# Kernel optimization log

Measured on AMD Instinct MI355X. Metric: run time of the kernel, lower is better.

## Reference

```python
import jax, jax.numpy as jnp
import numpy as np

D = 512
F = 2048
H = 8
L = 128
B = 4


def _layer_norm(x, g, b, eps=1e-5):
    mu = jnp.mean(x, axis=-1, keepdims=True)
    var = jnp.var(x, axis=-1, keepdims=True)
    return (x - mu) * jax.lax.rsqrt(var + eps) * g + b


def _edge_mlp(Q, arc, W, b, arc_is_middle_out):
    # Equivalent to relu(Linear(concat(A, arc, B_))) with W: (3D, D), without
    # materializing the (B,L,L,3D) concat: split W into three D-blocks.
    # For W_out: concat(h_bf, arc, h_bf_t) -> block1 acts on Q[b,i], block3 on Q[b,j].
    # For W_in:  concat(h_bf_t, arc, h_bf) -> block1 acts on Q[b,j], block3 on Q[b,i].
    d = Q.shape[-1]
    W1, W2, W3 = W[:d], W[d:2 * d], W[2 * d:]
    mid = jnp.einsum('bijd,de->bije', arc, W2)
    if arc_is_middle_out:  # W_out ordering
        left = jnp.einsum('bid,de->bie', Q, W1)[:, :, None, :]   # broadcast over j
        right = jnp.einsum('bjd,de->bje', Q, W3)[:, None, :, :]  # broadcast over i
    else:  # W_in ordering
        left = jnp.einsum('bjd,de->bje', Q, W1)[:, None, :, :]
        right = jnp.einsum('bid,de->bie', Q, W3)[:, :, None, :]
    return jax.nn.relu(left + mid + right + b)


def _gat_attn(Q, KV, q_w, q_b, k_w, k_b, v_w, v_b, o_w, o_b):
    # Edge-conditioned multihead attention: per-query K/V of shape (B,L,L,D).
    bsz, seq, d = Q.shape
    dh = d // H
    scale = dh ** -0.5
    q = ((Q @ q_w + q_b) * scale).reshape(bsz, seq, H, dh)
    k = (KV @ k_w + k_b).reshape(bsz, seq, seq, H, dh)
    v = (KV @ v_w + v_b).reshape(bsz, seq, seq, H, dh)
    scores = jnp.einsum('bihd,bijhd->bhij', q, k)
    attn = jax.nn.softmax(scores, axis=-1)
    out = jnp.einsum('bhij,bijhd->bihd', attn, v).reshape(bsz, seq, d)
    return out @ o_w + o_b


def setup_inputs() -> dict:
    key = jax.random.key(0)
    ks = jax.random.split(key, 24)
    s = 0.02
    inp = {
        'h': jax.random.normal(ks[0], (L, B, D), jnp.float32),
        'src_outcoming_arc_x': jax.random.normal(ks[1], (B, L, L, D), jnp.float32),
        'src_incoming_arc_x': jax.random.normal(ks[2], (B, L, L, D), jnp.float32),
        'encoder_padding_mask': jnp.zeros((B, L), jnp.bool_),
        'W_out_w': jax.random.normal(ks[3], (3 * D, D), jnp.float32) * s,
        'W_out_b': jnp.zeros((D,), jnp.float32),
        'W_in_w': jax.random.normal(ks[4], (3 * D, D), jnp.float32) * s,
        'W_in_b': jnp.zeros((D,), jnp.float32),
        'q_w': jax.random.normal(ks[5], (D, D), jnp.float32) * s,
        'q_b': jnp.zeros((D,), jnp.float32),
        'k_w': jax.random.normal(ks[6], (D, D), jnp.float32) * s,
        'k_b': jnp.zeros((D,), jnp.float32),
        'v_w': jax.random.normal(ks[7], (D, D), jnp.float32) * s,
        'v_b': jnp.zeros((D,), jnp.float32),
        'o_w': jax.random.normal(ks[8], (D, D), jnp.float32) * s,
        'o_b': jnp.zeros((D,), jnp.float32),
        'ln1_g': jnp.ones((D,), jnp.float32),
        'ln1_b': jnp.zeros((D,), jnp.float32),
        'fc1_w': jax.random.normal(ks[9], (D, F), jnp.float32) * s,
        'fc1_b': jnp.zeros((F,), jnp.float32),
        'fc2_w': jax.random.normal(ks[10], (F, D), jnp.float32) * s,
        'fc2_b': jnp.zeros((D,), jnp.float32),
        'ln2_g': jnp.ones((D,), jnp.float32),
        'ln2_b': jnp.zeros((D,), jnp.float32),
    }
    return inp


def reference(h, src_outcoming_arc_x, src_incoming_arc_x, encoder_padding_mask,
              W_out_w, W_out_b, W_in_w, W_in_b,
              q_w, q_b, k_w, k_b, v_w, v_b, o_w, o_b,
              ln1_g, ln1_b, fc1_w, fc1_b, fc2_w, fc2_b, ln2_g, ln2_b):
    # h: (L, B, D). Dropouts are identity (eval). attn_mask=None.
    residual = h
    Q = jnp.transpose(h, (1, 0, 2))  # (B, L, D)
    U_out = _edge_mlp(Q, src_outcoming_arc_x, W_out_w, W_out_b, True)
    att_out = _gat_attn(Q, U_out, q_w, q_b, k_w, k_b, v_w, v_b, o_w, o_b)
    U_in = _edge_mlp(Q, src_incoming_arc_x, W_in_w, W_in_b, False)
    att_in = _gat_attn(Q, U_in, q_w, q_b, k_w, k_b, v_w, v_b, o_w, o_b)
    x = jnp.transpose(att_in + att_out, (1, 0, 2))  # back to (L, B, D)
    x = _layer_norm(residual + x, ln1_g, ln1_b)
    residual = x
    x = jax.nn.relu(x @ fc1_w + fc1_b) @ fc2_w + fc2_b
    x = _layer_norm(residual + x, ln2_g, ln2_b)
    return x
```

## Files before the change

kernel.cpp:

```cpp
#include <hip/hip_runtime.h>
#include <stdint.h>
#include <stddef.h>

#define NTOK 512
#define NM   65536

typedef __bf16 bf16x8 __attribute__((ext_vector_type(8)));
typedef float  f32x4  __attribute__((ext_vector_type(4)));
typedef unsigned int u32x4 __attribute__((ext_vector_type(4)));

__device__ __forceinline__ unsigned short f2bf(float f) {
    unsigned int u = __builtin_bit_cast(unsigned int, f);
    u += 0x7FFFu + ((u >> 16) & 1u);
    return (unsigned short)(u >> 16);
}
__device__ __forceinline__ float bf2f(unsigned short s) {
    unsigned int u = ((unsigned int)s) << 16;
    return __builtin_bit_cast(float, u);
}

__device__ __forceinline__ void gload16(const void* g, void* l) {
    __builtin_amdgcn_global_load_lds(
        (const __attribute__((address_space(1))) void*)g,
        (__attribute__((address_space(3))) void*)l,
        16, 0, 0);
}

struct TRJob { const float* src; unsigned short* dst; int srcLd, dstLd, tcols; float scale; };
struct PrepArgs {
    const float* h; unsigned short* Qm;
    const float* kw; float* kwT;
    const float* Wob; const float* Wib; const float* qb; float* bias1;
    TRJob j[11]; int start[12];
};

__global__ __launch_bounds__(256) void k_prepAll(PrepArgs a) {
    __shared__ float tile[64][65];
    int bid = blockIdx.x;
    int t = threadIdx.x;
    if (bid < 1024) {
        int idx = bid * 256 + t;
        int tok = idx >> 9, d = idx & 511;
        int b = tok >> 7, i = tok & 127;
        a.Qm[idx] = f2bf(a.h[(i * 4 + b) * 512 + d]);
        return;
    } else if (bid < 2048) {
        int idx = (bid - 1024) * 256 + t;
        a.kwT[idx] = a.kw[(size_t)(idx & 511) * 512 + (idx >> 9)];
        return;
    } else if (bid < 2058) {
        int i = (bid - 2048) * 256 + t;
        if (i < 2560) {
            float v = 0.f;
            if (i < 512) v = a.Wob[i];
            else if (i < 1024) v = 0.f;
            else if (i < 1536) v = a.Wib[i - 1024];
            else if (i < 2048) v = 0.f;
            else v = a.qb[i - 2048] * 0.125f;
            a.bias1[i] = v;
        }
        return;
    }
    int b = bid - 2058;
    int ji = 0;
    while (ji < 10 && b >= a.start[ji + 1]) ++ji;
    TRJob jb = a.j[ji];
    int rel = b - a.start[ji];
    int bx = rel % jb.tcols, by = rel / jb.tcols;
    int r0 = by * 64, c0 = bx * 64;
    int c = t & 63, rr = t >> 6;
    #pragma unroll
    for (int ii = 0; ii < 16; ++ii) {
        int r = ii * 4 + rr;
        tile[r][c] = jb.src[(size_t)(r0 + r) * jb.srcLd + c0 + c];
    }
    __syncthreads();
    #pragma unroll
    for (int ii = 0; ii < 16; ++ii) {
        int n = ii * 4 + rr;
        jb.dst[(size_t)(c0 + n) * jb.dstLd + r0 + c] = f2bf(tile[c][n] * jb.scale);
    }
}

struct MMP {
    const unsigned short* A;  int lda;
    const float* Af2a; const float* Af2b; int ldaf;
    const unsigned short* Bt; int ldb;
    const float* bias;
    const float* accs;
    float* outF;
    unsigned short* outB;
    int ldo;
    int K;
    int relu;
    int aOffPerN64;
    int zKOff;
    int zOutOff;
    float biasScale;
};

__global__ __launch_bounds__(256) void k_mm(MMP p) {
    __shared__ unsigned char As[64 * 128];
    __shared__ unsigned char Bs[64 * 128];
    int t = threadIdx.x;
    int lane = t & 63, w = t >> 6;
    int m0 = blockIdx.x * 64, n0 = blockIdx.y * 64;
    int z = blockIdx.z;
    size_t aoffel = (size_t)(n0 >> 6) * p.aOffPerN64 + (size_t)z * p.zKOff;
    const unsigned short* A  = p.A + aoffel;
    const unsigned short* Bt = p.Bt + (size_t)z * p.zKOff;
    int wm = (w >> 1) * 32, wn = (w & 1) * 32;
    f32x4 acc[2][2];
    #pragma unroll
    for (int a = 0; a < 2; ++a)
        #pragma unroll
        for (int b = 0; b < 2; ++b) acc[a][b] = (f32x4){0.f, 0.f, 0.f, 0.f};

    for (int kb = 0; kb < p.K; kb += 64) {
        __syncthreads();
        #pragma unroll
        for (int s = 0; s < 2; ++s) {
            int c = t + s * 256;
            int r = c >> 3, kc = (c & 7) * 8;
            int off = (r * 128 + kc * 2) ^ ((r & 7) << 4);
            if (p.Af2a) {
                size_t ro = aoffel + (size_t)(m0 + r) * p.ldaf + kb + kc;
                const float4* xa = reinterpret_cast<const float4*>(p.Af2a + ro);
                const float4* ya = reinterpret_cast<const float4*>(p.Af2b + ro);
                float4 x0 = xa[0], x1 = xa[1], y0 = ya[0], y1 = ya[1];
                bf16x8 bv;
                bv[0] = (__bf16)(x0.x + y0.x); bv[1] = (__bf16)(x0.y + y0.y);
                bv[2] = (__bf16)(x0.z + y0.z); bv[3] = (__bf16)(x0.w + y0.w);
                bv[4] = (__bf16)(x1.x + y1.x); bv[5] = (__bf16)(x1.y + y1.y);
                bv[6] = (__bf16)(x1.z + y1.z); bv[7] = (__bf16)(x1.w + y1.w);
                *reinterpret_cast<bf16x8*>(As + off) = bv;
            } else {
                *reinterpret_cast<u32x4*>(As + off) =
                    *reinterpret_cast<const u32x4*>(A + (size_t)(m0 + r) * p.lda + kb + kc);
            }
            *reinterpret_cast<u32x4*>(Bs + off) =
                *reinterpret_cast<const u32x4*>(Bt + (size_t)(n0 + r) * p.ldb + kb + kc);
        }
        __syncthreads();
        #pragma unroll
        for (int kh = 0; kh < 2; ++kh) {
            int kk = kh * 32 + (lane >> 4) * 8;
            bf16x8 af[2], bfr[2];
            #pragma unroll
            for (int mf = 0; mf < 2; ++mf) {
                int r = wm + mf * 16 + (lane & 15);
                int off = (r * 128 + kk * 2) ^ ((r & 7) << 4);
                af[mf] = *reinterpret_cast<const bf16x8*>(As + off);
            }
            #pragma unroll
            for (int nf = 0; nf < 2; ++nf) {
                int r = wn + nf * 16 + (lane & 15);
                int off = (r * 128 + kk * 2) ^ ((r & 7) << 4);
                bfr[nf] = *reinterpret_cast<const bf16x8*>(Bs + off);
            }
            #pragma unroll
            for (int mf = 0; mf < 2; ++mf)
                #pragma unroll
                for (int nf = 0; nf < 2; ++nf)
                    acc[mf][nf] = __builtin_amdgcn_mfma_f32_16x16x32_bf16(
                        af[mf], bfr[nf], acc[mf][nf], 0, 0, 0);
        }
    }
    #pragma unroll
    for (int mf = 0; mf < 2; ++mf) {
        #pragma unroll
        for (int rr = 0; rr < 4; ++rr) {
            int gm = m0 + wm + mf * 16 + (lane >> 4) * 4 + rr;
            #pragma unroll
            for (int nf = 0; nf < 2; ++nf) {
                int e = n0 + wn + nf * 16 + (lane & 15);
                float v = acc[mf][nf][rr];
                if (p.bias) v += p.bias[e] * p.biasScale;
                if (p.relu) v = fmaxf(v, 0.f);
                if (p.accs) v += p.accs[(size_t)gm * p.ldo + e];
                size_t oo = (size_t)gm * p.ldo + e + (size_t)z * p.zOutOff;
                if (p.outF) p.outF[oo] = v;
                if (p.outB) p.outB[oo] = f2bf(v);
            }
        }
    }
}

__global__ __launch_bounds__(256) void k_prep2(const float* __restrict__ qs, int qld,
                                               const float* __restrict__ kwT,
                                               const float* __restrict__ k_b,
                                               unsigned short* __restrict__ p,
                                               float* __restrict__ c) {
    __shared__ float q8[8][512];
    int t = threadIdx.x;
    int tok0 = blockIdx.x * 8;
    int d = blockIdx.y * 256 + t;
    for (int idx = t; idx < 4096; idx += 256) {
        int s = idx >> 9, dd = idx & 511;
        q8[s][dd] = qs[(size_t)(tok0 + s) * qld + dd];
    }
    __syncthreads();
    if (blockIdx.y == 0 && t < 64) {
        int s = t >> 3, hh = t & 7;
        float cv = 0.f;
        for (int dh = 0; dh < 64; ++dh) cv += k_b[hh * 64 + dh] * q8[s][hh * 64 + dh];
        c[(tok0 + s) * 8 + hh] = cv;
    }
    for (int hh = 0; hh < 8; ++hh) {
        float pv[8];
        #pragma unroll
        for (int s = 0; s < 8; ++s) pv[s] = 0.f;
        for (int dh = 0; dh < 64; ++dh) {
            float wv = kwT[(size_t)(hh * 64 + dh) * 512 + d];
            #pragma unroll
            for (int s = 0; s < 8; ++s) pv[s] += wv * q8[s][hh * 64 + dh];
        }
        #pragma unroll
        for (int s = 0; s < 8; ++s)
            p[((size_t)(tok0 + s) * 8 + hh) * 512 + d] = f2bf(pv[s]);
    }
}

__global__ __launch_bounds__(256) void k_midU(const float* __restrict__ arcO,
                                              const float* __restrict__ arcI,
                                              const unsigned short* __restrict__ W2to,
                                              const unsigned short* __restrict__ W2ti,
                                              const float* __restrict__ QWcat,
                                              unsigned short* __restrict__ U0,
                                              unsigned short* __restrict__ U1) {
    __shared__ float As4[128 * 64];
    __shared__ unsigned short Bs2[128 * 64];
    int t = threadIdx.x;
    int lane = t & 63;
    int w = t >> 6;
    int bid = blockIdx.x;
    int xcd = bid & 7, slot = bid >> 3;
    int mtf = xcd * 128 + (slot >> 2);
    int nt = slot & 3;
    int arc01 = mtf >> 9;
    int mt = mtf & 511;
    const float* arc = arc01 ? arcI : arcO;
    const unsigned short* W2t = arc01 ? W2ti : W2to;
    const float* fixedMat = QWcat + (arc01 ? 1536 : 0);
    const float* rowMat   = QWcat + (arc01 ? 1024 : 512);
    unsigned short* U = arc01 ? U1 : U0;
    int m0 = mt * 128;
    int n0 = nt * 128;
    int wm = (w >> 1) * 64, wn = (w & 1) * 64;
    f32x4 acc[4][4];
    #pragma unroll
    for (int a = 0; a < 4; ++a)
        #pragma unroll
        for (int bq = 0; bq < 4; ++bq) acc[a][bq] = (f32x4){0.f, 0.f, 0.f, 0.f};

    int arA = lane >> 4;
    int acb = lane & 15;
    int brB = lane >> 3;
    int bcb = lane & 7;
    int ph0 = nt * 2;

    for (int s8 = 0; s8 < 8; ++s8) {
        int kb = (((s8 + ph0) & 7)) * 64;
        __syncthreads();
        #pragma unroll
        for (int i = 0; i < 8; ++i) {
            int base = (w * 8 + i) * 1024;
            int r = ((w * 8 + i) << 2) + arA;
            int cs = acb ^ (r & 7);
            gload16(arc + (size_t)(m0 + r) * 512 + kb + cs * 4,
                    (char*)As4 + base);
        }
        #pragma unroll
        for (int i = 0; i < 4; ++i) {
            int base = (w * 4 + i) * 1024;
            int r = ((w * 4 + i) << 3) + brB;
            int cs = bcb ^ (r & 7);
            gload16(W2t + (size_t)(n0 + r) * 512 + kb + cs * 8,
                    (char*)Bs2 + base);
        }
        __syncthreads();
        #pragma unroll
        for (int kh = 0; kh < 2; ++kh) {
            int kk = kh * 32 + (lane >> 4) * 8;
            bf16x8 af[4], bfr[4];
            #pragma unroll
            for (int mf = 0; mf < 4; ++mf) {
                int rr = wm + mf * 16 + (lane & 15);
                int c0 = kk >> 2;
                const char* bp = (const char*)As4 + rr * 256;
                float4 a0 = *reinterpret_cast<const float4*>(bp + ((c0 ^ (rr & 7)) << 4));
                float4 a1 = *reinterpret_cast<const float4*>(bp + (((c0 + 1) ^ (rr & 7)) << 4));
                af[mf][0] = (__bf16)a0.x; af[mf][1] = (__bf16)a0.y;
                af[mf][2] = (__bf16)a0.z; af[mf][3] = (__bf16)a0.w;
                af[mf][4] = (__bf16)a1.x; af[mf][5] = (__bf16)a1.y;
                af[mf][6] = (__bf16)a1.z; af[mf][7] = (__bf16)a1.w;
            }
            #pragma unroll
            for (int nf = 0; nf < 4; ++nf) {
                int rn = wn + nf * 16 + (lane & 15);
                int c = kk >> 3;
                bfr[nf] = *reinterpret_cast<const bf16x8*>(
                    (const char*)Bs2 + rn * 128 + ((c ^ (rn & 7)) << 4));
            }
            #pragma unroll
            for (int mf = 0; mf < 4; ++mf)
                #pragma unroll
                for (int nf = 0; nf < 4; ++nf)
                    acc[mf][nf] = __builtin_amdgcn_mfma_f32_16x16x32_bf16(
                        af[mf], bfr[nf], acc[mf][nf], 0, 0, 0);
        }
    }
    int tokI = mt;
    int bb = mt >> 7;
    float fx[4];
    #pragma unroll
    for (int nf = 0; nf < 4; ++nf)
        fx[nf] = fixedMat[(size_t)tokI * 2560 + n0 + wn + nf * 16 + (lane & 15)];
    #pragma unroll
    for (int mf = 0; mf < 4; ++mf) {
        #pragma unroll
        for (int r = 0; r < 4; ++r) {
            int row = wm + mf * 16 + (lane >> 4) * 4 + r;
            int gm = m0 + row;
            int tokJ = bb * 128 + (gm & 127);
            const float* rv = rowMat + (size_t)tokJ * 2560;
            #pragma unroll
            for (int nf = 0; nf < 4; ++nf) {
                int e = n0 + wn + nf * 16 + (lane & 15);
                float v = acc[mf][nf][r] + fx[nf] + rv[e];
                v = fmaxf(v, 0.f);
                U[(size_t)gm * 512 + e] = f2bf(v);
            }
        }
    }
}

__global__ __launch_bounds__(256) void k_att2(const unsigned short* __restrict__ U0,
                                              const unsigned short* __restrict__ U1,
                                              const unsigned short* __restrict__ p,
                                              const float* __restrict__ c,
                                              float* __restrict__ Wsum0,
                                              float* __restrict__ Wsum1) {
    __shared__ float at[8][128];
    int bid = blockIdx.x;
    int arc01 = bid >> 9;
    int tok = bid & 511;
    const unsigned short* U = arc01 ? U1 : U0;
    float* Ws = arc01 ? Wsum1 : Wsum0;
    int t = threadIdx.x;
    int w = t >> 6;
    int lane = t & 63;
    int hh = lane & 15;
    int kg = lane >> 4;
    bool hv = hh < 8;
    f32x4 acc[2];
    acc[0] = (f32x4){0.f, 0.f, 0.f, 0.f};
    acc[1] = (f32x4){0.f, 0.f, 0.f, 0.f};
    const unsigned short* Ub0 = U + (size_t)tok * 65536;
    const unsigned short* Ub = Ub0 + (size_t)(w * 32) * 512;
    const unsigned short* pb = p + ((size_t)tok * 8 + (hh & 7)) * 512;
    for (int ks = 0; ks < 16; ++ks) {
        int kcol = ks * 32 + kg * 8;
        u32x4 braw = (u32x4){0u, 0u, 0u, 0u};
        if (hv) braw = *reinterpret_cast<const u32x4*>(pb + kcol);
        bf16x8 bfrag = __builtin_bit_cast(bf16x8, braw);
        #pragma unroll
        for (int mf = 0; mf < 2; ++mf) {
            bf16x8 afrag = *reinterpret_cast<const bf16x8*>(
                Ub + (size_t)(mf * 16 + hh) * 512 + kcol);
            acc[mf] = __builtin_amdgcn_mfma_f32_16x16x32_bf16(afrag, bfrag, acc[mf], 0, 0, 0);
        }
    }
    if (hv) {
        float cval = c[tok * 8 + hh];
        #pragma unroll
        for (int mf = 0; mf < 2; ++mf)
            #pragma unroll
            for (int r = 0; r < 4; ++r)
                at[hh][w * 32 + mf * 16 + kg * 4 + r] = acc[mf][r] + cval;
    }
    __syncthreads();
    {
        int h2 = t >> 5, l32 = t & 31;
        float v0 = at[h2][l32], v1 = at[h2][l32 + 32],
              v2 = at[h2][l32 + 64], v3 = at[h2][l32 + 96];
        float mx = fmaxf(fmaxf(v0, v1), fmaxf(v2, v3));
        #pragma unroll
        for (int o = 16; o >= 1; o >>= 1) mx = fmaxf(mx, __shfl_xor(mx, o));
        float e0 = __expf(v0 - mx), e1 = __expf(v1 - mx),
              e2 = __expf(v2 - mx), e3 = __expf(v3 - mx);
        float sum = e0 + e1 + e2 + e3;
        #pragma unroll
        for (int o = 16; o >= 1; o >>= 1) sum += __shfl_xor(sum, o);
        float inv = 1.f / sum;
        at[h2][l32]      = e0 * inv;
        at[h2][l32 + 32] = e1 * inv;
        at[h2][l32 + 64] = e2 * inv;
        at[h2][l32 + 96] = e3 * inv;
    }
    __syncthreads();
    int d0 = t * 2;
    float a8[8][2];
    #pragma unroll
    for (int q = 0; q < 8; ++q) { a8[q][0] = 0.f; a8[q][1] = 0.f; }
    for (int j = 0; j < 128; ++j) {
        unsigned int uv = *reinterpret_cast<const unsigned int*>(Ub0 + (size_t)j * 512 + d0);
        float u0 = bf2f((unsigned short)(uv & 0xffffu));
        float u1 = bf2f((unsigned short)(uv >> 16));
        #pragma unroll
        for (int q = 0; q < 8; ++q) {
            float a = at[q][j];
            a8[q][0] += a * u0;
            a8[q][1] += a * u1;
        }
    }
    #pragma unroll
    for (int q = 0; q < 8; ++q) {
        size_t woff = ((size_t)tok * 8 + q) * 512 + d0;
        Ws[woff] = a8[q][0];
        Ws[woff + 1] = a8[q][1];
    }
}

__global__ __launch_bounds__(256) void k_ln(const float* __restrict__ A,
                                            const float* __restrict__ Bv, int bswap,
                                            const float* __restrict__ parts,
                                            const float* __restrict__ pbias,
                                            const float* __restrict__ g,
                                            const float* __restrict__ bta,
                                            float* __restrict__ outF,
                                            unsigned short* __restrict__ outB) {
    int t = threadIdx.x;
    int tok = blockIdx.x;
    size_t aoff = (size_t)tok * 512;
    float b0, b1;
    if (parts) {
        b0 = parts[aoff + t] + parts[262144 + aoff + t] +
             parts[524288 + aoff + t] + parts[786432 + aoff + t] + pbias[t];
        b1 = parts[aoff + t + 256] + parts[262144 + aoff + t + 256] +
             parts[524288 + aoff + t + 256] + parts[786432 + aoff + t + 256] + pbias[t + 256];
    } else {
        size_t boff = aoff;
        if (bswap) { int i = tok >> 2, b = tok & 3; boff = (size_t)(b * 128 + i) * 512; }
        b0 = Bv[boff + t];
        b1 = Bv[boff + t + 256];
    }
    float v0 = A[aoff + t] + b0;
    float v1 = A[aoff + t + 256] + b1;
    float s = v0 + v1, q = v0 * v0 + v1 * v1;
    #pragma unroll
    for (int o = 32; o >= 1; o >>= 1) { s += __shfl_xor(s, o); q += __shfl_xor(q, o); }
    __shared__ float red[8];
    int w = t >> 6, lane = t & 63;
    if (lane == 0) { red[w] = s; red[4 + w] = q; }
    __syncthreads();
    float ts = red[0] + red[1] + red[2] + red[3];
    float tq = red[4] + red[5] + red[6] + red[7];
    float mean = ts * (1.f / 512.f);
    float var = tq * (1.f / 512.f) - mean * mean;
    float inv = rsqrtf(var + 1e-5f);
    float o0 = (v0 - mean) * inv * g[t] + bta[t];
    float o1 = (v1 - mean) * inv * g[t + 256] + bta[t + 256];
    outF[aoff + t] = o0;
    outF[aoff + t + 256] = o1;
    if (outB) { outB[aoff + t] = f2bf(o0); outB[aoff + t + 256] = f2bf(o1); }
}

extern "C" void kernel_launch(void* const* d_in, const int* in_sizes, int n_in,
                              void* d_out, int out_size, void* d_ws, size_t ws_size,
                              hipStream_t stream) {
    (void)in_sizes; (void)n_in; (void)out_size; (void)ws_size;
    const float* h       = (const float*)d_in[0];
    const float* arc_out = (const float*)d_in[1];
    const float* arc_in  = (const float*)d_in[2];
    const float* W_out_w = (const float*)d_in[4];
    const float* W_out_b = (const float*)d_in[5];
    const float* W_in_w  = (const float*)d_in[6];
    const float* W_in_b  = (const float*)d_in[7];
    const float* q_w  = (const float*)d_in[8];
    const float* q_b  = (const float*)d_in[9];
    const float* k_w  = (const float*)d_in[10];
    const float* k_b  = (const float*)d_in[11];
    const float* v_w  = (const float*)d_in[12];
    const float* v_b  = (const float*)d_in[13];
    const float* o_w  = (const float*)d_in[14];
    const float* o_b  = (const float*)d_in[15];
    const float* ln1_g = (const float*)d_in[16];
    const float* ln1_b = (const float*)d_in[17];
    const float* fc1_w = (const float*)d_in[18];
    const float* fc1_b = (const float*)d_in[19];
    const float* fc2_w = (const float*)d_in[20];
    const float* fc2_b = (const float*)d_in[21];
    const float* ln2_g = (const float*)d_in[22];
    const float* ln2_b = (const float*)d_in[23];
    float* out = (float*)d_out;

    char* wsb = (char*)d_ws;
    size_t off = 0;
    auto ALLOC = [&](size_t bytes) -> void* {
        void* ptr = wsb + off;
        off += (bytes + 255) & ~(size_t)255;
        return ptr;
    };
    unsigned short* WcatT = (unsigned short*)ALLOC((size_t)2560 * 512 * 2);
    unsigned short* W2to  = (unsigned short*)ALLOC(262144 * 2);
    unsigned short* W2ti  = (unsigned short*)ALLOC(262144 * 2);
    unsigned short* o_wT  = (unsigned short*)ALLOC(262144 * 2);
    unsigned short* v_wT  = (unsigned short*)ALLOC(262144 * 2);
    unsigned short* fc1T  = (unsigned short*)ALLOC((size_t)2048 * 512 * 2);
    unsigned short* fc2T  = (unsigned short*)ALLOC((size_t)512 * 2048 * 2);
    float* kwT   = (float*)ALLOC(262144 * 4);
    float* bias1 = (float*)ALLOC(2560 * 4);
    unsigned short* Qm = (unsigned short*)ALLOC(262144 * 2);
    float* QWcat = (float*)ALLOC((size_t)512 * 2560 * 4);
    unsigned short* pbuf = (unsigned short*)ALLOC((size_t)NTOK * 8 * 512 * 2);
    float* cbuf = (float*)ALLOC(NTOK * 8 * 4);
    unsigned short* Ubuf0 = (unsigned short*)ALLOC((size_t)NM * 512 * 2);
    unsigned short* Ubuf1 = (unsigned short*)ALLOC((size_t)NM * 512 * 2);
    float* Wsum0 = (float*)ALLOC((size_t)NTOK * 8 * 512 * 4);
    float* Wsum1 = (float*)ALLOC((size_t)NTOK * 8 * 512 * 4);
    unsigned short* tmpb  = (unsigned short*)ALLOC(262144 * 2);
    float* attsum = (float*)ALLOC(262144 * 4);
    float* x1  = (float*)ALLOC(262144 * 4);
    unsigned short* x1b = (unsigned short*)ALLOC(262144 * 2);
    unsigned short* ybb = (unsigned short*)ALLOC((size_t)NTOK * 2048 * 2);
    float* zparts = (float*)ALLOC((size_t)4 * 262144 * 4);

    {
        PrepArgs a = {};
        a.h = h; a.Qm = Qm; a.kw = k_w; a.kwT = kwT;
        a.Wob = W_out_b; a.Wib = W_in_b; a.qb = q_b; a.bias1 = bias1;
        auto SET = [&](int i, const float* s, int sld, unsigned short* d, int dld,
                       float sc, int tiles, int tcols) {
            a.j[i] = TRJob{s, d, sld, dld, tcols, sc};
            a.start[i + 1] = a.start[i] + tiles;
        };
        a.start[0] = 0;
        SET(0,  W_out_w,              512, WcatT,              512, 1.f,    64, 8);
        SET(1,  W_out_w + 1024 * 512, 512, WcatT + 512 * 512,  512, 1.f,    64, 8);
        SET(2,  W_in_w,               512, WcatT + 1024 * 512, 512, 1.f,    64, 8);
        SET(3,  W_in_w + 1024 * 512,  512, WcatT + 1536 * 512, 512, 1.f,    64, 8);
        SET(4,  q_w,                  512, WcatT + 2048 * 512, 512, 0.125f, 64, 8);
        SET(5,  W_out_w + 512 * 512,  512, W2to,               512, 1.f,    64, 8);
        SET(6,  W_in_w + 512 * 512,   512, W2ti,               512, 1.f,    64, 8);
        SET(7,  o_w,                  512, o_wT,               512, 1.f,    64, 8);
        SET(8,  v_w,                  512, v_wT,               512, 1.f,    64, 8);
        SET(9,  fc1_w,               2048, fc1T,               512, 1.f,   256, 32);
        SET(10, fc2_w,                512, fc2T,              2048, 1.f,   256, 8);
        k_prepAll<<<2058 + a.start[11], 256, 0, stream>>>(a);
    }

    {
        MMP m = {};
        m.A = Qm; m.lda = 512; m.Bt = WcatT; m.ldb = 512;
        m.bias = bias1; m.biasScale = 1.f;
        m.outF = QWcat; m.ldo = 2560; m.K = 512;
        k_mm<<<dim3(8, 40), 256, 0, stream>>>(m);
    }
    k_prep2<<<dim3(64, 2), 256, 0, stream>>>(QWcat + 2048, 2560, kwT, k_b, pbuf, cbuf);

    k_midU<<<4096, 256, 0, stream>>>(arc_out, arc_in, W2to, W2ti, QWcat, Ubuf0, Ubuf1);
    k_att2<<<1024, 256, 0, stream>>>(Ubuf0, Ubuf1, pbuf, cbuf, Wsum0, Wsum1);

    {
        MMP m = {};
        m.Af2a = Wsum0; m.Af2b = Wsum1; m.ldaf = 4096; m.aOffPerN64 = 512;
        m.A = (const unsigned short*)Wsum0;
        m.Bt = v_wT; m.ldb = 512;
        m.bias = v_b; m.biasScale = 2.f;
        m.outB = tmpb; m.ldo = 512; m.K = 512;
        k_mm<<<dim3(8, 8), 256, 0, stream>>>(m);
    }
    {
        MMP m = {};
        m.A = tmpb; m.lda = 512; m.Bt = o_wT; m.ldb = 512;
        m.bias = o_b; m.biasScale = 2.f;
        m.outF = attsum; m.ldo = 512; m.K = 512;
        k_mm<<<dim3(8, 8), 256, 0, stream>>>(m);
    }

    k_ln<<<512, 256, 0, stream>>>(h, attsum, 1, nullptr, nullptr, ln1_g, ln1_b, x1, x1b);

    {
        MMP m = {};
        m.A = x1b; m.lda = 512; m.Bt = fc1T; m.ldb = 512;
        m.bias = fc1_b; m.biasScale = 1.f;
        m.relu = 1; m.outB = ybb; m.ldo = 2048; m.K = 512;
        k_mm<<<dim3(8, 32), 256, 0, stream>>>(m);
    }
    {
        MMP m = {};
        m.A = ybb; m.lda = 2048; m.Bt = fc2T; m.ldb = 2048;
        m.outF = zparts; m.ldo = 512; m.K = 512;
        m.zKOff = 512; m.zOutOff = 262144;
        k_mm<<<dim3(8, 8, 4), 256, 0, stream>>>(m);
    }
    k_ln<<<512, 256, 0, stream>>>(x1, nullptr, 0, zparts, fc2_b, ln2_g, ln2_b, out, nullptr);
}
```

Measured before the change: 339.5 us.

## Prefetch arc tile into registers and store as bf16 in LDS

The k_midU GEMM now loads the fp32 arc A-tile through registers instead of direct global-to-LDS loads. The next k-step is prefetched into registers during the MFMA loop, and the tile is converted to bf16 once before it is written to LDS. This halves the A-tile LDS footprint and read traffic, and removes the repeated per-wave fp32-to-bf16 conversion in the inner loop. The cost is higher register pressure, and the per-block k-phase rotation that spread out concurrent accesses to the same W2 columns is removed.

```diff
diff --git a/kernel.cpp b/kernel.cpp
--- a/kernel.cpp
+++ b/kernel.cpp
@@ -228,7 +228,7 @@
                                               const float* __restrict__ QWcat,
                                               unsigned short* __restrict__ U0,
                                               unsigned short* __restrict__ U1) {
-    __shared__ float As4[128 * 64];
+    __shared__ unsigned short As2[128 * 64];
     __shared__ unsigned short Bs2[128 * 64];
     int t = threadIdx.x;
     int lane = t & 63;
@@ -253,32 +253,51 @@
         #pragma unroll
         for (int bq = 0; bq < 4; ++bq) acc[a][bq] = (f32x4){0.f, 0.f, 0.f, 0.f};
 
-    int arA = lane >> 4;
-    int acb = lane & 15;
+    int r0t = t >> 3, ct = t & 7;
     int brB = lane >> 3;
     int bcb = lane & 7;
-    int ph0 = nt * 2;
-
+    float4 pA0[4], pA1[4];
+
+#define ALOAD(KB)                                                               \
+    _Pragma("unroll")                                                           \
+    for (int j = 0; j < 4; ++j) {                                               \
+        int r = r0t + 32 * j;                                                   \
+        const float* ga = arc + (size_t)(m0 + r) * 512 + (KB) + ct * 8;         \
+        pA0[j] = *reinterpret_cast<const float4*>(ga);                          \
+        pA1[j] = *reinterpret_cast<const float4*>(ga + 4);                      \
+    }
+
+#define AWRITE()                                                                \
+    _Pragma("unroll")                                                           \
+    for (int j = 0; j < 4; ++j) {                                               \
+        int r = r0t + 32 * j;                                                   \
+        int off = (r * 128 + ct * 16) ^ ((r & 7) << 4);                         \
+        bf16x8 bv;                                                              \
+        bv[0] = (__bf16)pA0[j].x; bv[1] = (__bf16)pA0[j].y;                     \
+        bv[2] = (__bf16)pA0[j].z; bv[3] = (__bf16)pA0[j].w;                     \
+        bv[4] = (__bf16)pA1[j].x; bv[5] = (__bf16)pA1[j].y;                     \
+        bv[6] = (__bf16)pA1[j].z; bv[7] = (__bf16)pA1[j].w;                     \
+        *reinterpret_cast<bf16x8*>((char*)As2 + off) = bv;                      \
+    }
+
+#define GLOADB(KB)                                                              \
+    _Pragma("unroll")                                                           \
+    for (int i = 0; i < 4; ++i) {                                               \
+        int base = (w * 4 + i) * 1024;                                          \
+        int r = ((w * 4 + i) << 3) + brB;                                       \
+        int cs = bcb ^ (r & 7);                                                 \
+        gload16(W2t + (size_t)(n0 + r) * 512 + (KB) + cs * 8,                   \
+                (char*)Bs2 + base);                                             \
+    }
+
+    ALOAD(0);
     for (int s8 = 0; s8 < 8; ++s8) {
-        int kb = (((s8 + ph0) & 7)) * 64;
+        int kb = s8 * 64;
         __syncthreads();
-        #pragma unroll
-        for (int i = 0; i < 8; ++i) {
-            int base = (w * 8 + i) * 1024;
-            int r = ((w * 8 + i) << 2) + arA;
-            int cs = acb ^ (r & 7);
-            gload16(arc + (size_t)(m0 + r) * 512 + kb + cs * 4,
-                    (char*)As4 + base);
-        }
-        #pragma unroll
-        for (int i = 0; i < 4; ++i) {
-            int base = (w * 4 + i) * 1024;
-            int r = ((w * 4 + i) << 3) + brB;
-            int cs = bcb ^ (r & 7);
-            gload16(W2t + (size_t)(n0 + r) * 512 + kb + cs * 8,
-                    (char*)Bs2 + base);
-        }
+        AWRITE();
+        GLOADB(kb);
         __syncthreads();
+        if (s8 < 7) { ALOAD(kb + 64); }
         #pragma unroll
         for (int kh = 0; kh < 2; ++kh) {
             int kk = kh * 32 + (lane >> 4) * 8;
@@ -286,14 +305,9 @@
             #pragma unroll
             for (int mf = 0; mf < 4; ++mf) {
                 int rr = wm + mf * 16 + (lane & 15);
-                int c0 = kk >> 2;
-                const char* bp = (const char*)As4 + rr * 256;
-                float4 a0 = *reinterpret_cast<const float4*>(bp + ((c0 ^ (rr & 7)) << 4));
-                float4 a1 = *reinterpret_cast<const float4*>(bp + (((c0 + 1) ^ (rr & 7)) << 4));
-                af[mf][0] = (__bf16)a0.x; af[mf][1] = (__bf16)a0.y;
-                af[mf][2] = (__bf16)a0.z; af[mf][3] = (__bf16)a0.w;
-                af[mf][4] = (__bf16)a1.x; af[mf][5] = (__bf16)a1.y;
-                af[mf][6] = (__bf16)a1.z; af[mf][7] = (__bf16)a1.w;
+                int c = kk >> 3;
+                af[mf] = *reinterpret_cast<const bf16x8*>(
+                    (const char*)As2 + ((rr * 128 + (c ^ (rr & 7)) * 16)));
             }
             #pragma unroll
             for (int nf = 0; nf < 4; ++nf) {
@@ -310,6 +324,9 @@
                         af[mf], bfr[nf], acc[mf][nf], 0, 0, 0);
         }
     }
+#undef ALOAD
+#undef AWRITE
+#undef GLOADB
     int tokI = mt;
     int bb = mt >> 7;
     float fx[4];
```

New measurement: 387.1 us. 14.0% more time.
